# Optimization experiments

Measured on AMD Instinct MI355X. Metric: run time of the kernel, lower is better.

## Reference

```python
import jax, jax.numpy as jnp
import numpy as np

HEIGHT = 0.1        # height_factor
MIN_DIST = 10       # min_distance
PROM = 0.05         # prominence_factor


def _find_peaks(xn):
    """scipy.signal.find_peaks(xn, height=HEIGHT, distance=MIN_DIST,
    prominence=PROM) for a single 1D signal, vectorized.
    (Plateau handling omitted: for continuous random inputs exact ties have
    probability zero, so strict local maxima match scipy's _local_maxima_1d.)"""
    N = xn.shape[0]
    pos = jnp.arange(N)

    # 1) strict local maxima (endpoints can never be peaks in scipy)
    interior = (xn[1:-1] > xn[:-2]) & (xn[1:-1] > xn[2:])
    is_peak = jnp.pad(interior, (1, 1), constant_values=False)

    # 2) height filter
    cand = is_peak & (xn >= HEIGHT)

    # 3) distance-based greedy suppression: highest peak first, remove
    #    neighbors with |i-j| < MIN_DIST (matches _select_by_peak_distance)
    order = jnp.argsort(-xn)  # descending by value

    def step(suppressed, idx):
        keep_this = cand[idx] & ~suppressed[idx]
        near = (jnp.abs(pos - idx) < MIN_DIST) & (pos != idx)
        suppressed = suppressed | (keep_this & near)
        return suppressed, keep_this

    _, keeps = jax.lax.scan(step, jnp.zeros(N, dtype=bool), order)
    keep = jnp.zeros(N, dtype=bool).at[order].set(keeps)

    # 4) prominence (wlen=None -> full-signal base search, per position):
    #    left base  = min x over (L, i] where L = last j<i with x[j] > x[i]
    #    right base = min x over [i, R) where R = first j>i with x[j] > x[i]
    greater = xn[None, :] > xn[:, None]              # [i, j]: x_j > x_i
    left_stop = greater & (pos[None, :] < pos[:, None])
    L = jnp.max(jnp.where(left_stop, pos[None, :], -1), axis=1)
    right_stop = greater & (pos[None, :] > pos[:, None])
    R = jnp.min(jnp.where(right_stop, pos[None, :], N), axis=1)

    big = jnp.asarray(jnp.inf, xn.dtype)
    in_l = (pos[None, :] > L[:, None]) & (pos[None, :] <= pos[:, None])
    lmin = jnp.min(jnp.where(in_l, xn[None, :], big), axis=1)
    in_r = (pos[None, :] >= pos[:, None]) & (pos[None, :] < R[:, None])
    rmin = jnp.min(jnp.where(in_r, xn[None, :], big), axis=1)
    prominence = xn - jnp.maximum(lmin, rmin)

    keep = keep & (prominence >= PROM)
    return keep.astype(xn.dtype)


def setup_inputs() -> dict:
    key = jax.random.key(0)
    x = jax.random.normal(key, (16, 2048), dtype=jnp.float32)
    return {"x": x}


def reference(x):
    # per-sample min-max normalization, as in the torch module
    xmin = jnp.min(x, axis=-1, keepdims=True)
    xmax = jnp.max(x, axis=-1, keepdims=True)
    xn = (x - xmin) / (xmax - xmin + 1e-5)
    return jax.vmap(_find_peaks)(xn)
```

## Files before the change

### kernel.cpp

```cpp
#include <hip/hip_runtime.h>

#define N 2048
#define NT 256
#define EL 8
#define HEIGHTF 0.1f
#define PROMF 0.05f
#define MD1 9
#define LVLS 8

__global__ __launch_bounds__(NT)
void peak_kernel(const float* __restrict__ x, float* __restrict__ out) {
    __shared__ float xs[N];
    __shared__ float actl[16 + N + 24];
    __shared__ unsigned int nk32[3 + NT + 3];
    __shared__ float TMX[LVLS][N];
    __shared__ float TMN[LVLS][N];
    __shared__ float wred[8];
    __shared__ int cont[2];
    __shared__ int wtot[4];
    __shared__ unsigned short klist[NT];
    __shared__ unsigned char keepres[N];

    const int row = blockIdx.x;
    const int t = threadIdx.x;
    const int base = t * EL;
    const float* xr = x + row * (size_t)N;
    const int wv = t >> 6, ln = t & 63;

    float4 Ld0 = ((const float4*)(xr + base))[0];
    float4 Ld1 = ((const float4*)(xr + base))[1];
    float v0[EL] = {Ld0.x, Ld0.y, Ld0.z, Ld0.w, Ld1.x, Ld1.y, Ld1.z, Ld1.w};
    float mn = v0[0], mx = v0[0];
    #pragma unroll
    for (int e = 1; e < EL; ++e) { mn = fminf(mn, v0[e]); mx = fmaxf(mx, v0[e]); }
    #pragma unroll
    for (int off = 32; off > 0; off >>= 1) {
        mn = fminf(mn, __shfl_xor(mn, off, 64));
        mx = fmaxf(mx, __shfl_xor(mx, off, 64));
    }
    if (ln == 0) { wred[wv] = mn; wred[4 + wv] = mx; }
    if (t == 0) {
        nk32[0] = 0; nk32[1] = 0; nk32[2] = 0;
        nk32[3+NT] = 0; nk32[3+NT+1] = 0; nk32[3+NT+2] = 0;
        cont[0] = 0;
    }
    if (t < 16) actl[t] = -1e30f;
    if (t < 24) actl[16 + N + t] = -1e30f;
    __syncthreads();

    const float xmin = fminf(fminf(wred[0], wred[1]), fminf(wred[2], wred[3]));
    const float xmax = fmaxf(fmaxf(wred[4], wred[5]), fmaxf(wred[6], wred[7]));
    const float den = (xmax - xmin) + 1e-5f;
    float vn[EL];
    #pragma unroll
    for (int e = 0; e < EL; ++e) {
        vn[e] = (v0[e] - xmin) / den;
        xs[base + e] = vn[e];
    }
    __syncthreads();

    unsigned int undec = 0, kept = 0;
    #pragma unroll
    for (int e = 0; e < EL; ++e) {
        int i = base + e;
        float v = vn[e];
        float lf = (e == 0) ? ((i >= 1) ? xs[i-1] : 3e38f) : vn[e-1];
        float rt = (e == EL-1) ? ((i+1 < N) ? xs[i+1] : 3e38f) : vn[e+1];
        bool c = (i >= 1) && (i <= N-2) && (v > lf) && (v > rt) && (v >= HEIGHTF);
        if (c) undec |= (1u << e);
        actl[16 + i] = c ? v : -1e30f;
    }
    __syncthreads();

    float a[40];
    {
        const float4* ap = (const float4*)(actl + base);
        #pragma unroll
        for (int q = 0; q < 10; ++q) {
            float4 w = ap[q];
            a[4*q+0] = w.x; a[4*q+1] = w.y; a[4*q+2] = w.z; a[4*q+3] = w.w;
        }
    }

    auto compute_wins = [&](unsigned int ud) -> unsigned int {
        float m2v[25], m4v[23], m8v[19];
        #pragma unroll
        for (int s = 0; s < 25; ++s) m2v[s] = fmaxf(a[7+s], a[8+s]);
        #pragma unroll
        for (int s = 0; s < 23; ++s) m4v[s] = fmaxf(m2v[s], m2v[s+2]);
        #pragma unroll
        for (int s = 0; s < 19; ++s) m8v[s] = fmaxf(m4v[s], m4v[s+4]);
        unsigned int wb = 0;
        #pragma unroll
        for (int e = 0; e < EL; ++e) {
            if (ud & (1u << e)) {
                float v = a[16+e];
                float wl = fmaxf(m8v[e], a[15+e]);
                float wr = fmaxf(m8v[10+e], a[25+e]);
                if (wl < v && wr <= v) wb |= (1u << e);
            }
        }
        return wb;
    };

    unsigned int winb = undec ? compute_wins(undec) : 0u;

    unsigned int* nkp = nk32 + 3;
    for (int round = 0; round < 2048; ++round) {
        nkp[t] = winb;
        if (t == 0) cont[(round + 1) & 1] = 0;
        if (undec) cont[round & 1] = 1;
        __syncthreads();
        if (cont[round & 1] == 0) break;
        unsigned long long V = 0;
        #pragma unroll
        for (int q = 0; q < 7; ++q)
            V |= ((unsigned long long)(nkp[t - 3 + q] & 0xFFu)) << (8 * q);
        V <<= 1;
        if (__ballot(V != 0ULL)) {
            #pragma unroll
            for (int e = 0; e < EL; ++e) {
                if (undec & (1u << e)) {
                    unsigned int w19 = (unsigned int)((V >> (16 + e)) & 0x7FFFFULL);
                    if (w19 & (1u << 9)) { kept |= (1u << e); undec &= ~(1u << e); }
                    else if (w19)        { undec &= ~(1u << e); }
                }
            }
            #pragma unroll
            for (int s = 0; s < 40; ++s) {
                if ((V >> s) & 0x7FFFFULL) a[s] = -1e30f;
            }
        }
        winb = 0;
        if (__ballot(undec != 0)) winb = compute_wins(undec);
    }

    float cx[EL], cn[EL];
    #pragma unroll
    for (int j = 0; j < EL; ++j) {
        int i = t + j * NT;
        float a0 = xs[i];
        bool inb = (i + 1 < N);
        float nb = inb ? xs[i + 1] : 0.0f;
        cx[j] = fmaxf(a0, inb ? nb : -3e38f);
        cn[j] = fminf(a0, inb ? nb : 3e38f);
        TMX[0][i] = cx[j];
        TMN[0][i] = cn[j];
    }
    int myc = __popc(kept);
    int pre = myc;
    #pragma unroll
    for (int off = 1; off < 64; off <<= 1) {
        int up = __shfl_up(pre, off, 64);
        if (ln >= off) pre += up;
    }
    if (ln == 63) wtot[wv] = pre;
    #pragma unroll
    for (int e = 0; e < EL; ++e) keepres[base + e] = 0;
    __syncthreads();

    {
        int woff = 0;
        #pragma unroll
        for (int w = 0; w < 4; ++w) woff += (w < wv) ? wtot[w] : 0;
        int slot = woff + pre - myc;
        #pragma unroll
        for (int e = 0; e < EL; ++e)
            if (kept & (1u << e)) klist[slot++] = (unsigned short)(base + e);
    }
    const int ktot = wtot[0] + wtot[1] + wtot[2] + wtot[3];
    for (int Lv = 1; Lv < LVLS; ++Lv) {
        int h = 1 << Lv;
        #pragma unroll
        for (int j = 0; j < EL; ++j) {
            int i = t + j * NT;
            bool inb = (i + h < N);
            float bx = inb ? TMX[Lv-1][i+h] : -3e38f;
            float bn = inb ? TMN[Lv-1][i+h] : 3e38f;
            cx[j] = fmaxf(cx[j], bx);
            cn[j] = fminf(cn[j], bn);
            TMX[Lv][i] = cx[j];
            TMN[Lv][i] = cn[j];
        }
        __syncthreads();
    }

    if (t < ktot) {
        const int i = klist[t];
        const float v = xs[i];
        float m = v;
        int p = i - 1;
        while (p >= 0) {
            int len = p + 1;
            int k = (len >= (1 << LVLS)) ? LVLS : (31 - __clz(len));
            int s = p + 1 - (1 << k);
            float wmx = (k == 0) ? xs[s] : TMX[k-1][s];
            if (wmx > v) {
                while (k > 0) {
                    int half = 1 << (k - 1);
                    int rs = s + half;
                    float rm = (k == 1) ? xs[rs] : TMX[k-2][rs];
                    if (rm > v) s = rs;
                    else m = fminf(m, (k == 1) ? xs[rs] : TMN[k-2][rs]);
                    --k;
                }
                break;
            } else {
                m = fminf(m, (k == 0) ? xs[s] : TMN[k-1][s]);
                p = s - 1;
            }
        }
        const float lmin = m;
        m = v;
        p = i + 1;
        while (p < N) {
            int len = N - p;
            int k = (len >= (1 << LVLS)) ? LVLS : (31 - __clz(len));
            float wmx = (k == 0) ? xs[p] : TMX[k-1][p];
            if (wmx > v) {
                while (k > 0) {
                    int half = 1 << (k - 1);
                    float lm = (k == 1) ? xs[p] : TMX[k-2][p];
                    if (!(lm > v)) {
                        m = fminf(m, (k == 1) ? xs[p] : TMN[k-2][p]);
                        p += half;
                    }
                    --k;
                }
                break;
            } else {
                m = fminf(m, (k == 0) ? xs[p] : TMN[k-1][p]);
                p += 1 << k;
            }
        }
        const float rmin = m;
        if (v - fmaxf(lmin, rmin) >= PROMF) keepres[i] = 1;
    }
    __syncthreads();

    float res[EL];
    #pragma unroll
    for (int e = 0; e < EL; ++e) res[e] = keepres[base + e] ? 1.0f : 0.0f;
    float* outr = out + row * (size_t)N + base;
    ((float4*)outr)[0] = make_float4(res[0], res[1], res[2], res[3]);
    ((float4*)outr)[1] = make_float4(res[4], res[5], res[6], res[7]);
}

extern "C" void kernel_launch(void* const* d_in, const int* in_sizes, int n_in,
                              void* d_out, int out_size, void* d_ws, size_t ws_size,
                              hipStream_t stream) {
    const float* x = (const float*)d_in[0];
    float* outp = (float*)d_out;
    const int rows = in_sizes[0] / N;
    peak_kernel<<<rows, NT, 0, stream>>>(x, outp);
}
```

Baseline: 24.26 us.

## Overlap sparse-table build with suppression rounds and add wave-level tail resolver

The sparse min/max table levels are now built one level per suppression round, so that work hides inside the iterative loop instead of running after it. The continue flag is replaced by __syncthreads_count. Once 16 or fewer threads still hold undecided candidates, those candidates are gathered, sorted by value in a single wave with a bitonic sort, and resolved greedily with ballots, which cuts the long tail of rounds. This adds atomics, extra barriers and more code complexity in the loop.

```diff
diff --git a/kernel.cpp b/kernel.cpp
--- a/kernel.cpp
+++ b/kernel.cpp
@@ -16,10 +16,11 @@
     __shared__ float TMX[LVLS][N];
     __shared__ float TMN[LVLS][N];
     __shared__ float wred[8];
-    __shared__ int cont[2];
     __shared__ int wtot[4];
     __shared__ unsigned short klist[NT];
     __shared__ unsigned char keepres[N];
+    __shared__ int scnt;
+    __shared__ unsigned short spos[128];
 
     const int row = blockIdx.x;
     const int t = threadIdx.x;
@@ -42,7 +43,7 @@
     if (t == 0) {
         nk32[0] = 0; nk32[1] = 0; nk32[2] = 0;
         nk32[3+NT] = 0; nk32[3+NT+1] = 0; nk32[3+NT+2] = 0;
-        cont[0] = 0;
+        scnt = 0;
     }
     if (t < 16) actl[t] = -1e30f;
     if (t < 24) actl[16 + N + t] = -1e30f;
@@ -70,6 +71,15 @@
         if (c) undec |= (1u << e);
         actl[16 + i] = c ? v : -1e30f;
     }
+    #pragma unroll
+    for (int j = 0; j < EL; ++j) {
+        int i = t + j * NT;
+        float a0 = xs[i];
+        bool inb = (i + 1 < N);
+        float nb = inb ? xs[i + 1] : 0.0f;
+        TMX[0][i] = fmaxf(a0, inb ? nb : -3e38f);
+        TMN[0][i] = fminf(a0, inb ? nb : 3e38f);
+    }
     __syncthreads();
 
     float a[40];
@@ -104,14 +114,14 @@
     };
 
     unsigned int winb = undec ? compute_wins(undec) : 0u;
-
     unsigned int* nkp = nk32 + 3;
-    for (int round = 0; round < 2048; ++round) {
+    int tb = 0;
+    bool done = false;
+
+    for (int round = 1; round <= 2048; ++round) {
         nkp[t] = winb;
-        if (t == 0) cont[(round + 1) & 1] = 0;
-        if (undec) cont[round & 1] = 1;
-        __syncthreads();
-        if (cont[round & 1] == 0) break;
+        int cnt = __syncthreads_count(undec != 0);
+        if (cnt == 0) break;
         unsigned long long V = 0;
         #pragma unroll
         for (int q = 0; q < 7; ++q)
@@ -127,26 +137,74 @@
                 }
             }
             #pragma unroll
-            for (int s = 0; s < 40; ++s) {
+            for (int s = 0; s < 40; ++s)
                 if ((V >> s) & 0x7FFFFULL) a[s] = -1e30f;
-            }
-        }
-        winb = 0;
-        if (__ballot(undec != 0)) winb = compute_wins(undec);
-    }
-
-    float cx[EL], cn[EL];
-    #pragma unroll
-    for (int j = 0; j < EL; ++j) {
-        int i = t + j * NT;
-        float a0 = xs[i];
-        bool inb = (i + 1 < N);
-        float nb = inb ? xs[i + 1] : 0.0f;
-        cx[j] = fmaxf(a0, inb ? nb : -3e38f);
-        cn[j] = fminf(a0, inb ? nb : 3e38f);
-        TMX[0][i] = cx[j];
-        TMN[0][i] = cn[j];
-    }
+        }
+        if (round < LVLS) {
+            int h = 1 << round;
+            #pragma unroll
+            for (int j = 0; j < EL; ++j) {
+                int i = t + j * NT;
+                bool inb = (i + h < N);
+                TMX[round][i] = fmaxf(TMX[round-1][i], inb ? TMX[round-1][i+h] : -3e38f);
+                TMN[round][i] = fminf(TMN[round-1][i], inb ? TMN[round-1][i+h] : 3e38f);
+            }
+            tb = round;
+        }
+        if (cnt <= 16) {
+            #pragma unroll
+            for (int e = 0; e < EL; ++e) {
+                if (undec & (1u << e)) {
+                    int s = atomicAdd(&scnt, 1);
+                    if (s < 128) spos[s] = (unsigned short)(base + e);
+                }
+            }
+            __syncthreads();
+            const int m = scnt;
+            nkp[t] = 0;
+            __syncthreads();
+            if (m > 0 && m <= 64) {
+                if (t < 64) {
+                    unsigned long long key = 0ULL;
+                    if (t < m) {
+                        int p0 = spos[t];
+                        key = ((unsigned long long)__float_as_uint(xs[p0]) << 32)
+                            | (unsigned long long)(unsigned)(N - 1 - p0);
+                    }
+                    #pragma unroll
+                    for (int k = 2; k <= 64; k <<= 1) {
+                        #pragma unroll
+                        for (int j = k >> 1; j > 0; j >>= 1) {
+                            unsigned long long other = __shfl_xor(key, j, 64);
+                            bool takeMax = (((ln & k) == 0) == ((ln & j) == 0));
+                            bool gt = key > other;
+                            key = (takeMax == gt) ? key : other;
+                        }
+                    }
+                    int sp = (int)(N - 1 - (int)(unsigned)(key & 0xFFFFFFFFULL));
+                    unsigned long long mask = __ballot(key != 0ULL);
+                    bool iwon = false;
+                    while (mask) {
+                        int L = __builtin_ctzll(mask);
+                        int lpos = __shfl(sp, L, 64);
+                        if (ln == L) iwon = true;
+                        unsigned long long nearm =
+                            __ballot(sp >= lpos - MD1 && sp <= lpos + MD1);
+                        mask &= ~nearm;
+                    }
+                    if (iwon) atomicOr(&nkp[sp >> 3], 1u << (sp & 7));
+                }
+            } else if (m > 64) {
+                if (t == 0) scnt = 0;
+            }
+            __syncthreads();
+            if (m == 0) done = true;
+            else if (m <= 64) { kept |= nkp[t]; undec = 0; done = true; }
+            if (done) break;
+        }
+        winb = (__ballot(undec != 0)) ? compute_wins(undec) : 0u;
+    }
+
     int myc = __popc(kept);
     int pre = myc;
     #pragma unroll
@@ -157,33 +215,30 @@
     if (ln == 63) wtot[wv] = pre;
     #pragma unroll
     for (int e = 0; e < EL; ++e) keepres[base + e] = 0;
-    __syncthreads();
-
-    {
-        int woff = 0;
-        #pragma unroll
-        for (int w = 0; w < 4; ++w) woff += (w < wv) ? wtot[w] : 0;
-        int slot = woff + pre - myc;
-        #pragma unroll
-        for (int e = 0; e < EL; ++e)
-            if (kept & (1u << e)) klist[slot++] = (unsigned short)(base + e);
-    }
-    const int ktot = wtot[0] + wtot[1] + wtot[2] + wtot[3];
-    for (int Lv = 1; Lv < LVLS; ++Lv) {
+    for (int Lv = tb + 1; Lv < LVLS; ++Lv) {
+        __syncthreads();
         int h = 1 << Lv;
         #pragma unroll
         for (int j = 0; j < EL; ++j) {
             int i = t + j * NT;
             bool inb = (i + h < N);
-            float bx = inb ? TMX[Lv-1][i+h] : -3e38f;
-            float bn = inb ? TMN[Lv-1][i+h] : 3e38f;
-            cx[j] = fmaxf(cx[j], bx);
-            cn[j] = fminf(cn[j], bn);
-            TMX[Lv][i] = cx[j];
-            TMN[Lv][i] = cn[j];
-        }
-        __syncthreads();
-    }
+            TMX[Lv][i] = fmaxf(TMX[Lv-1][i], inb ? TMX[Lv-1][i+h] : -3e38f);
+            TMN[Lv][i] = fminf(TMN[Lv-1][i], inb ? TMN[Lv-1][i+h] : 3e38f);
+        }
+    }
+    __syncthreads();
+
+    {
+        int woff = 0;
+        #pragma unroll
+        for (int w = 0; w < 4; ++w) woff += (w < wv) ? wtot[w] : 0;
+        int slot = woff + pre - myc;
+        #pragma unroll
+        for (int e = 0; e < EL; ++e)
+            if (kept & (1u << e)) klist[slot++] = (unsigned short)(base + e);
+    }
+    const int ktot = wtot[0] + wtot[1] + wtot[2] + wtot[3];
+    __syncthreads();
 
     if (t < ktot) {
         const int i = klist[t];
```

New measurement: 26.61 us. +9.7%, slower.
